# Kernel tuning notes

Hardware: AMD Instinct MI355X
Metric: run time of the kernel (lower is better)

Reference implementation:

```python
import jax, jax.numpy as jnp
import numpy as np

N = 50000   # nodes
E = 800000  # edges (avg degree 16)
F = 16      # input node feature dim
H = 64      # hidden_channels
G = 128     # number of graphs
L = 3       # num_layers
OUT = 8     # output_channels


def _glorot(key, shape):
    fan = shape[-2] + shape[-1]
    return jax.random.normal(key, shape, dtype=jnp.float32) * jnp.sqrt(2.0 / fan)


def setup_inputs() -> dict:
    key = jax.random.key(0)
    ks = jax.random.split(key, 16)
    z = lambda *s: jnp.zeros(s, jnp.float32)
    return {
        "x": jax.random.normal(ks[0], (N, F), jnp.float32),
        "pos": jax.random.normal(ks[1], (N, 3), jnp.float32),
        "edge_index": jax.random.randint(ks[2], (2, E), 0, N),
        "batch": jnp.sort(jax.random.randint(ks[3], (N,), 0, G)),
        "node_W1": _glorot(ks[4], (F, H)), "node_b1": z(H),
        "node_W2": _glorot(ks[5], (H, H)), "node_b2": z(H),
        "local_W1": _glorot(ks[6], (L, 2 * H + 3, H)), "local_b1": z(L, H),
        "local_W2": _glorot(ks[7], (L, H, H)), "local_b2": z(L, H),
        "global_W1": _glorot(ks[8], (L, H, H)), "global_b1": z(L, H),
        "global_W2": _glorot(ks[9], (L, H, H)), "global_b2": z(L, H),
        "lin1_W": _glorot(ks[10], (H, H // 2)), "lin1_b": z(H // 2),
        "lin2_W": _glorot(ks[11], (H // 2, OUT)), "lin2_b": z(OUT),
    }


def reference(x, pos, edge_index, batch,
              node_W1, node_b1, node_W2, node_b2,
              local_W1, local_b1, local_W2, local_b2,
              global_W1, global_b1, global_W2, global_b2,
              lin1_W, lin1_b, lin2_W, lin2_b):
    n = x.shape[0]
    src, dst = edge_index[0], edge_index[1]  # x_j = x[src], x_i = x[dst]
    # node_lin: Linear -> ReLU -> Linear
    h = jnp.maximum(x @ node_W1 + node_b1, 0.0) @ node_W2 + node_b2
    for l in range(L):
        # message: cat([x_i, x_j, pos_j]) -> local_nn (Linear, ReLU, Linear)
        m = jnp.concatenate([h[dst], h[src], pos[src]], axis=-1)  # [E, 2H+3]
        m = jnp.maximum(m @ local_W1[l] + local_b1[l], 0.0) @ local_W2[l] + local_b2[l]
        # aggregate: scatter-add over destination nodes
        agg = jax.ops.segment_sum(m, dst, num_segments=n)
        # global_nn (Linear, ReLU, Linear), then outer ReLU from forward loop
        h = jnp.maximum(agg @ global_W1[l] + global_b1[l], 0.0) @ global_W2[l] + global_b2[l]
        h = jnp.maximum(h, 0.0)
    h = jnp.maximum(h @ lin1_W + lin1_b, 0.0)
    out = h @ lin2_W + lin2_b  # [N, OUT]
    # graph readout: scatter-add over batch ids
    return jax.ops.segment_sum(out, batch, num_segments=G)  # [G, OUT]
```

## Files before the change

kernel.cpp:

```cpp
#include <hip/hip_runtime.h>

#define N_NODES 50000
#define N_EDGES 800000
#define NGRAPH  128
#define XPITCH  72
#define NB      391
#define HEPB    4096
#define SEPB    8192
#define NGRP    3125
#define STRIDE  64
#define SENT    N_NODES

typedef short bf16x8 __attribute__((ext_vector_type(8)));
typedef float f32x4  __attribute__((ext_vector_type(4)));


__device__ __forceinline__ float atomAddF(float* p, float v) {
#if defined(__gfx950__) || defined(__AMDGCN__)
    return unsafeAtomicAdd(p, v);
#else
    return atomicAdd(p, v);
#endif
}

__device__ __forceinline__ unsigned short f2bf(float x) {
    unsigned u = __builtin_bit_cast(unsigned, x);
    u += 0x7fffu + ((u >> 16) & 1u);
    return (unsigned short)(u >> 16);
}
__device__ __forceinline__ float bf2f(unsigned short h) {
    return __builtin_bit_cast(float, (unsigned)h << 16);
}

__device__ __forceinline__ f32x4 mk4(float b) { f32x4 a = {b, b, b, b}; return a; }

template<int NKC, int KROW>
__device__ __forceinline__ f32x4 w_tile(const bf16x8* a,
                                        const unsigned short* __restrict__ Wm,
                                        int nt, int col, int quad, f32x4 acc) {
    const unsigned short* wp = Wm + (nt * 16 + col) * KROW + quad * 8;
#pragma unroll
    for (int c = 0; c < NKC; ++c) {
        bf16x8 b = *(const bf16x8*)(wp + c * 32);
        acc = __builtin_amdgcn_mfma_f32_16x16x32_bf16(a[c], b, acc, 0, 0, 0);
    }
    return acc;
}

template<int NKC>
__device__ __forceinline__ void a_load(const unsigned short* __restrict__ sl,
                                       int col, int quad, bf16x8* a) {
    a[0] = *(const bf16x8*)(sl + col * XPITCH + quad * 8);
    if (NKC > 1) a[1] = *(const bf16x8*)(sl + col * XPITCH + quad * 8 + 32);
}

__device__ __forceinline__ void w_store1(unsigned short* __restrict__ sl,
                                         int wv, int col, int quad, f32x4 acc,
                                         bool relu) {
#pragma unroll
    for (int r = 0; r < 4; ++r) {
        float x = acc[r];
        if (relu) x = fmaxf(x, 0.f);
        sl[(quad * 4 + r) * XPITCH + wv * 16 + col] = f2bf(x);
    }
}

__device__ __forceinline__ void g_store1(unsigned short* __restrict__ g, int gn0,
                                         int wv, int col, int quad, f32x4 acc) {
#pragma unroll
    for (int r = 0; r < 4; ++r) {
        int node = gn0 + quad * 4 + r;
        if (node < N_NODES)
            g[(size_t)node * 64 + wv * 16 + col] = f2bf(acc[r]);
    }
}

__device__ __forceinline__ void wave_agg4(const int* dg, unsigned short* __restrict__ sl,
                                          const unsigned short* __restrict__ u,
                                          const unsigned short* __restrict__ vin,
                                          const unsigned short* __restrict__ srcList,
                                          int gn0, int wv, int lane) {
    int sub = lane & 15, q = lane >> 4;
    int n0 = gn0 + wv * 4;
    ushort4 uu4[4];
#pragma unroll
    for (int mi = 0; mi < 4; ++mi)
        uu4[mi] = *(const ushort4*)(u + (size_t)(n0 + mi) * 64 + sub * 4);

#pragma unroll
    for (int mi = 0; mi < 4; ++mi) {
        int m = wv * 4 + mi;
        float u0 = bf2f(uu4[mi].x), u1 = bf2f(uu4[mi].y);
        float u2 = bf2f(uu4[mi].z), u3 = bf2f(uu4[mi].w);
        int pdeg = (dg[m] + 15) & ~15;
        size_t b = (size_t)(n0 + mi) * STRIDE;
        float a0 = 0.f, a1 = 0.f, a2 = 0.f, a3 = 0.f;

        for (int g0 = 0; g0 < pdeg; g0 += 16) {
            ushort4 ss = *(const ushort4*)(srcList + b + g0 + 4 * q);
            int s0 = ss.x, s1 = ss.y, s2 = ss.z, s3 = ss.w;
            ushort4 w0 = *(const ushort4*)(vin + (size_t)s0 * 64 + sub * 4);
            ushort4 w1 = *(const ushort4*)(vin + (size_t)s1 * 64 + sub * 4);
            ushort4 w2 = *(const ushort4*)(vin + (size_t)s2 * 64 + sub * 4);
            ushort4 w3 = *(const ushort4*)(vin + (size_t)s3 * 64 + sub * 4);
            a0 += fmaxf(u0 + bf2f(w0.x), 0.f) + fmaxf(u0 + bf2f(w1.x), 0.f)
                + fmaxf(u0 + bf2f(w2.x), 0.f) + fmaxf(u0 + bf2f(w3.x), 0.f);
            a1 += fmaxf(u1 + bf2f(w0.y), 0.f) + fmaxf(u1 + bf2f(w1.y), 0.f)
                + fmaxf(u1 + bf2f(w2.y), 0.f) + fmaxf(u1 + bf2f(w3.y), 0.f);
            a2 += fmaxf(u2 + bf2f(w0.z), 0.f) + fmaxf(u2 + bf2f(w1.z), 0.f)
                + fmaxf(u2 + bf2f(w2.z), 0.f) + fmaxf(u2 + bf2f(w3.z), 0.f);
            a3 += fmaxf(u3 + bf2f(w0.w), 0.f) + fmaxf(u3 + bf2f(w1.w), 0.f)
                + fmaxf(u3 + bf2f(w2.w), 0.f) + fmaxf(u3 + bf2f(w3.w), 0.f);
        }

        a0 += __shfl_xor(a0, 16); a0 += __shfl_xor(a0, 32);
        a1 += __shfl_xor(a1, 16); a1 += __shfl_xor(a1, 32);
        a2 += __shfl_xor(a2, 16); a2 += __shfl_xor(a2, 32);
        a3 += __shfl_xor(a3, 16); a3 += __shfl_xor(a3, 32);

        if (q == 0) {
            ushort4 o;
            o.x = f2bf(a0); o.y = f2bf(a1); o.z = f2bf(a2); o.w = f2bf(a3);
            *(ushort4*)&sl[m * XPITCH + sub * 4] = o;
        }
    }
}

#define OFF_NW1T  0
#define OFF_NW2T  2048
#define OFF_LYR   6144
#define LYR_SZ    20480
#define OFF_LIN1T 67584
#define OFF_LIN2T 69632
#define WT_TOTAL  70144

__global__ __launch_bounds__(256) void kPrep(
    const float* __restrict__ nW1, const float* __restrict__ nW2,
    const float* __restrict__ lW1, const float* __restrict__ lW2,
    const float* __restrict__ gW1, const float* __restrict__ gW2,
    const float* __restrict__ lin1W, const float* __restrict__ lin2W,
    unsigned short* __restrict__ WT, int* __restrict__ gHist,
    int* __restrict__ doneCnt, float* __restrict__ out,
    unsigned short* __restrict__ v0, unsigned short* __restrict__ v1) {
    int i = blockIdx.x * 256 + threadIdx.x;
    if (blockIdx.x == 0) {
        for (int k = threadIdx.x; k < NB; k += 256) gHist[k] = 0;
        for (int k = threadIdx.x; k < NGRAPH * 8; k += 256) out[k] = 0.f;
        if (threadIdx.x == 0) *doneCnt = 0;
    }
    if (i < 64) {
        v0[(size_t)N_NODES * 64 + i] = 0xFF80;
        v1[(size_t)N_NODES * 64 + i] = 0xFF80;
    }
    if (i >= WT_TOTAL) return;
    int j = i;
    if (j < 2048) {
        int n = j >> 5, k = j & 31;
        WT[i] = (k < 16) ? f2bf(nW1[k * 64 + n]) : 0;
        return;
    }
    j -= 2048;
    if (j < 4096) {
        int n = j >> 6, k = j & 63;
        WT[i] = f2bf(nW2[k * 64 + n]);
        return;
    }
    j -= 4096;
    if (j < 3 * LYR_SZ) {
        int l = j / LYR_SZ;  j -= l * LYR_SZ;
        int m = j >> 12;     j &= 4095;
        int n = j >> 6, k = j & 63;
        const float* src;
        if (m == 0)      src = lW1 + (size_t)l * 131 * 64;
        else if (m == 1) src = lW1 + (size_t)l * 131 * 64 + 64 * 64;
        else if (m == 2) src = lW2 + (size_t)l * 4096;
        else if (m == 3) src = gW1 + (size_t)l * 4096;
        else             src = gW2 + (size_t)l * 4096;
        WT[i] = f2bf(src[k * 64 + n]);
        return;
    }
    j -= 3 * LYR_SZ;
    if (j < 2048) {
        int n = j >> 6, k = j & 63;
        WT[i] = f2bf(lin1W[k * 32 + n]);
        return;
    }
    j -= 2048;
    {
        int n = j >> 5, k = j & 31;
        WT[i] = (n < 8) ? f2bf(lin2W[k * 8 + n]) : 0;
    }
}

__global__ __launch_bounds__(256) void kHist(const int* __restrict__ ei,
                                             int* __restrict__ gHist,
                                             int* __restrict__ bucketOff,
                                             int* __restrict__ cursor,
                                             int* __restrict__ doneCnt) {
    __shared__ int h[NB];
    __shared__ int s0[512], s1[512];
    __shared__ int amLast;
    int tid = threadIdx.x;
    for (int i = tid; i < NB; i += 256) h[i] = 0;
    __syncthreads();
    int base = blockIdx.x * HEPB;
#pragma unroll
    for (int k = 0; k < HEPB; k += 256) {
        int e = base + k + tid;
        if (e < N_EDGES) atomicAdd(&h[ei[N_EDGES + e] >> 7], 1);
    }
    __syncthreads();
    for (int i = tid; i < NB; i += 256)
        if (h[i]) atomicAdd(&gHist[i], h[i]);

    __threadfence();
    if (tid == 0) amLast = (atomicAdd(doneCnt, 1) == (int)gridDim.x - 1);
    __syncthreads();
    if (!amLast) return;
    __threadfence();

    for (int e = tid; e < 512; e += 256)
        s0[e] = (e < NB) ? atomicAdd(&gHist[e], 0) : 0;
    __syncthreads();
    int* sp = s0; int* dp = s1;
    for (int off = 1; off < 512; off <<= 1) {
        for (int e = tid; e < 512; e += 256)
            dp[e] = sp[e] + ((e >= off) ? sp[e - off] : 0);
        __syncthreads();
        int* t = sp; sp = dp; dp = t;
    }
    for (int e = tid; e < NB; e += 256) {
        int cnt = atomicAdd(&gHist[e], 0);
        int excl = sp[e] - cnt;
        bucketOff[e] = excl;
        cursor[e] = excl;
    }
    if (tid == 0) bucketOff[NB] = sp[NB - 1];
}

__global__ __launch_bounds__(256) void kScat(const int* __restrict__ ei,
                                             int* __restrict__ cursor,
                                             int* __restrict__ packs) {
    __shared__ int sdata[SEPB];
    __shared__ int hist[NB];
    __shared__ int loff[NB + 1];
    __shared__ int gbase[NB];
    __shared__ int sc0[512], sc1[512];
    int tid = threadIdx.x;
    int base = blockIdx.x * SEPB;
    int nE = min(SEPB, N_EDGES - base);

    for (int i = tid; i < NB; i += 256) hist[i] = 0;
    __syncthreads();

    int myPack[SEPB / 256];
    unsigned short myRank[SEPB / 256];
#pragma unroll
    for (int kk = 0; kk < SEPB / 256; ++kk) {
        int e = base + kk * 256 + tid;
        if (e < N_EDGES) {
            int s = ei[e], d = ei[N_EDGES + e];
            myPack[kk] = (s << 16) | d;
            myRank[kk] = (unsigned short)atomicAdd(&hist[d >> 7], 1);
        }
    }
    __syncthreads();

    for (int e = tid; e < 512; e += 256) sc0[e] = (e < NB) ? hist[e] : 0;
    __syncthreads();
    int* sp = sc0; int* dp = sc1;
    for (int off = 1; off < 512; off <<= 1) {
        for (int e = tid; e < 512; e += 256)
            dp[e] = sp[e] + ((e >= off) ? sp[e - off] : 0);
        __syncthreads();
        int* t = sp; sp = dp; dp = t;
    }
    for (int e = tid; e < NB; e += 256) loff[e] = sp[e] - hist[e];
    if (tid == 0) loff[NB] = sp[NB - 1];
    __syncthreads();

    for (int e = tid; e < NB; e += 256)
        gbase[e] = hist[e] ? atomicAdd(&cursor[e], hist[e]) : 0;
#pragma unroll
    for (int kk = 0; kk < SEPB / 256; ++kk) {
        int e = base + kk * 256 + tid;
        if (e < N_EDGES) {
            int p = myPack[kk];
            int b = (p & 0xffff) >> 7;
            sdata[loff[b] + myRank[kk]] = p;
        }
    }
    __syncthreads();

    for (int i = tid; i < nE; i += 256) {
        int p = sdata[i];
        int b = (p & 0xffff) >> 7;
        packs[gbase[b] + (i - loff[b])] = p;
    }
}

__global__ __launch_bounds__(256) void kSortA(
    const int* __restrict__ bucketOff, const int* __restrict__ packs,
    unsigned short* __restrict__ srcList, int* __restrict__ degArr,
    const float* __restrict__ x, const float* __restrict__ pos,
    const unsigned short* __restrict__ WT,
    const float* __restrict__ nb1, const float* __restrict__ nb2,
    const float* __restrict__ lW1f, const float* __restrict__ lb1,
    unsigned short* __restrict__ u, unsigned short* __restrict__ v) {
    __shared__ int cur[128];
    __shared__ unsigned short SL[16 * XPITCH];
    __shared__ float pw[48];

    int tid = threadIdx.x;
    if (blockIdx.x < NB) {
        int nbk = blockIdx.x;
        int nodeBase = nbk * 128;
        int nvalid = min(128, N_NODES - nodeBase);
        int eb = bucketOff[nbk], ee = bucketOff[nbk + 1];

        if (tid < 128) cur[tid] = 0;
        __syncthreads();
        for (int i = eb + tid; i < ee; i += 256) {
            int p = packs[i];
            int node = p & 127;
            int r = atomicAdd(&cur[node], 1);
            if (r < STRIDE)
                srcList[(size_t)(nodeBase + node) * STRIDE + r] =
                    (unsigned short)(((unsigned)p) >> 16);
        }
        __syncthreads();
        if (tid < nvalid) {
            int d = min(cur[tid], STRIDE);
            degArr[nodeBase + tid] = d;
            int pd = (d + 15) & ~15;
            size_t b2 = (size_t)(nodeBase + tid) * STRIDE;
            for (int r = d; r < pd; ++r) srcList[b2 + r] = (unsigned short)SENT;
        }
        return;
    }

    int gn0 = (blockIdx.x - NB) * 16;
    int lane = tid & 63;
    int wv = __builtin_amdgcn_readfirstlane(tid >> 6);
    int col = lane & 15, quad = lane >> 4;

    for (int idx = tid; idx < 512; idx += 256) {
        int m = idx >> 5, k = idx & 31;
        int node = gn0 + m;
        float val = (k < 16) ? x[(size_t)node * 16 + k] : 0.f;
        SL[m * XPITCH + k] = f2bf(val);
    }
    if (tid < 48) {
        int node = gn0 + tid / 3;
        pw[tid] = pos[(size_t)node * 3 + tid % 3];
    }
    __syncthreads();

    bf16x8 a[2];
    f32x4 acc;

    a_load<1>(SL, col, quad, a);
    acc = w_tile<1, 32>(a, WT + OFF_NW1T, wv, col, quad, mk4(nb1[wv * 16 + col]));
    __syncthreads();
    w_store1(SL, wv, col, quad, acc, true);
    __syncthreads();

    a_load<2>(SL, col, quad, a);
    acc = w_tile<2, 64>(a, WT + OFF_NW2T, wv, col, quad, mk4(nb2[wv * 16 + col]));
    __syncthreads();
    w_store1(SL, wv, col, quad, acc, false);
    __syncthreads();

    const unsigned short* aT = WT + OFF_LYR;
    const unsigned short* bT = aT + 4096;
    const float* W1c = lW1f + 128 * 64;

    a_load<2>(SL, col, quad, a);
    acc = w_tile<2, 64>(a, aT, wv, col, quad, mk4(0.f));
    g_store1(u, gn0, wv, col, quad, acc);

    int ch = wv * 16 + col;
    acc = w_tile<2, 64>(a, bT, wv, col, quad, mk4(lb1[ch]));
    float w0 = W1c[ch], w1 = W1c[64 + ch], w2 = W1c[128 + ch];
#pragma unroll
    for (int r = 0; r < 4; ++r) {
        int rr = quad * 4 + r;
        acc[r] += pw[rr * 3 + 0] * w0 + pw[rr * 3 + 1] * w1 + pw[rr * 3 + 2] * w2;
    }
    g_store1(v, gn0, wv, col, quad, acc);
}

__global__ __launch_bounds__(256) void kB(
    const float* __restrict__ pos, const int* __restrict__ degArr,
    const unsigned short* __restrict__ srcList,
    const unsigned short* __restrict__ WT, int l,
    const float* __restrict__ lb2, const float* __restrict__ gb1,
    const float* __restrict__ gb2,
    const float* __restrict__ lW1f_next, const float* __restrict__ b1n,
    unsigned short* __restrict__ u,
    const unsigned short* __restrict__ vin,
    unsigned short* __restrict__ vout) {
    __shared__ unsigned short SL[16 * XPITCH];
    __shared__ float pw[48];
    __shared__ int dgW[16];
    int tid = threadIdx.x;
    int lane = tid & 63;
    int wv = __builtin_amdgcn_readfirstlane(tid >> 6);
    int gn0 = blockIdx.x * 16;
    int col = lane & 15, quad = lane >> 4;

    const unsigned short* LYR = WT + OFF_LYR + (size_t)l * LYR_SZ;
    const unsigned short* lW2T = LYR + 2 * 4096;
    const unsigned short* gW1T = LYR + 3 * 4096;
    const unsigned short* gW2T = LYR + 4 * 4096;
    const unsigned short* aTn = WT + OFF_LYR + (size_t)(l + 1) * LYR_SZ;
    const unsigned short* bTn = aTn + 4096;

    if (tid < 48) {
        int node = gn0 + tid / 3;
        pw[tid] = pos[(size_t)node * 3 + tid % 3];
    }
    if (tid < 16) dgW[tid] = degArr[gn0 + tid];
    __syncthreads();

    wave_agg4(dgW, SL, u, vin, srcList, gn0, wv, lane);
    __syncthreads();

    bf16x8 a[2];
    f32x4 acc;
    float dgr[4];
#pragma unroll
    for (int r = 0; r < 4; ++r) dgr[r] = (float)dgW[quad * 4 + r];

    {
        float b = lb2[wv * 16 + col];
        f32x4 init = {dgr[0] * b, dgr[1] * b, dgr[2] * b, dgr[3] * b};
        a_load<2>(SL, col, quad, a);
        acc = w_tile<2, 64>(a, lW2T, wv, col, quad, init);
    }
    __syncthreads();
    w_store1(SL, wv, col, quad, acc, false);
    __syncthreads();

    a_load<2>(SL, col, quad, a);
    acc = w_tile<2, 64>(a, gW1T, wv, col, quad, mk4(gb1[wv * 16 + col]));
    __syncthreads();
    w_store1(SL, wv, col, quad, acc, true);
    __syncthreads();

    a_load<2>(SL, col, quad, a);
    acc = w_tile<2, 64>(a, gW2T, wv, col, quad, mk4(gb2[wv * 16 + col]));
    __syncthreads();
    w_store1(SL, wv, col, quad, acc, true);
    __syncthreads();

    a_load<2>(SL, col, quad, a);
    acc = w_tile<2, 64>(a, aTn, wv, col, quad, mk4(0.f));
    g_store1(u, gn0, wv, col, quad, acc);

    const float* W1c = lW1f_next + 128 * 64;
    int ch = wv * 16 + col;
    acc = w_tile<2, 64>(a, bTn, wv, col, quad, mk4(b1n[ch]));
    float w0 = W1c[ch], w1 = W1c[64 + ch], w2 = W1c[128 + ch];
#pragma unroll
    for (int r = 0; r < 4; ++r) {
        int rr = quad * 4 + r;
        acc[r] += pw[rr * 3 + 0] * w0 + pw[rr * 3 + 1] * w1 + pw[rr * 3 + 2] * w2;
    }
    g_store1(vout, gn0, wv, col, quad, acc);
}

__global__ __launch_bounds__(256) void kC(
    const int* __restrict__ degArr, const unsigned short* __restrict__ srcList,
    const int* __restrict__ batch, const unsigned short* __restrict__ WT,
    const float* __restrict__ lb2, const float* __restrict__ gb1,
    const float* __restrict__ gb2,
    const float* __restrict__ lin1b, const float* __restrict__ lin2b,
    const unsigned short* __restrict__ u, const unsigned short* __restrict__ vin,
    float* __restrict__ out) {
    __shared__ unsigned short SL[16 * XPITCH];
    __shared__ int dgW[16];
    __shared__ int batchW[16];
    __shared__ float bins[16 * 8];
    int tid = threadIdx.x;
    int lane = tid & 63;
    int wv = __builtin_amdgcn_readfirstlane(tid >> 6);
    int gn0 = blockIdx.x * 16;
    int col = lane & 15, quad = lane >> 4;

    const unsigned short* LYR = WT + OFF_LYR + 2 * LYR_SZ;
    const unsigned short* lW2T = LYR + 2 * 4096;
    const unsigned short* gW1T = LYR + 3 * 4096;
    const unsigned short* gW2T = LYR + 4 * 4096;
    const unsigned short* lin1T = WT + OFF_LIN1T;
    const unsigned short* lin2T = WT + OFF_LIN2T;

    if (tid < 16) dgW[tid] = degArr[gn0 + tid];
    if (tid >= 32 && tid < 48) batchW[tid - 32] = batch[gn0 + tid - 32];
    if (tid >= 128 && tid < 256) bins[tid - 128] = 0.f;
    __syncthreads();

    wave_agg4(dgW, SL, u, vin, srcList, gn0, wv, lane);
    __syncthreads();

    bf16x8 a[2];
    f32x4 acc;
    float dgr[4];
#pragma unroll
    for (int r = 0; r < 4; ++r) dgr[r] = (float)dgW[quad * 4 + r];

    {
        float b = lb2[wv * 16 + col];
        f32x4 init = {dgr[0] * b, dgr[1] * b, dgr[2] * b, dgr[3] * b};
        a_load<2>(SL, col, quad, a);
        acc = w_tile<2, 64>(a, lW2T, wv, col, quad, init);
    }
    __syncthreads();
    w_store1(SL, wv, col, quad, acc, false);
    __syncthreads();

    a_load<2>(SL, col, quad, a);
    acc = w_tile<2, 64>(a, gW1T, wv, col, quad, mk4(gb1[wv * 16 + col]));
    __syncthreads();
    w_store1(SL, wv, col, quad, acc, true);
    __syncthreads();

    a_load<2>(SL, col, quad, a);
    acc = w_tile<2, 64>(a, gW2T, wv, col, quad, mk4(gb2[wv * 16 + col]));
    __syncthreads();
    w_store1(SL, wv, col, quad, acc, true);
    __syncthreads();

    a_load<2>(SL, col, quad, a);
    if (wv < 2)
        acc = w_tile<2, 64>(a, lin1T, wv, col, quad, mk4(lin1b[wv * 16 + col]));
    __syncthreads();
    if (wv < 2) w_store1(SL, wv, col, quad, acc, true);
    __syncthreads();

    if (wv == 0) {
        a_load<1>(SL, col, quad, a);
        f32x4 o = w_tile<1, 32>(a, lin2T, 0, col, quad,
                                mk4(col < 8 ? lin2b[col] : 0.f));
        int gmin = batchW[0];
        if (col < 8) {
#pragma unroll
            for (int r = 0; r < 4; ++r) {
                int nl = quad * 4 + r;
                atomicAdd(&bins[(batchW[nl] - gmin) * 8 + col], o[r]);
            }
        }
    }
    __syncthreads();
    int gmin = batchW[0];
    int nb8 = (batchW[15] - gmin + 1) * 8;
    for (int idx = tid; idx < nb8; idx += 256)
        atomAddF(&out[gmin * 8 + idx], bins[idx]);
}

extern "C" void kernel_launch(void* const* d_in, const int* in_sizes, int n_in,
                              void* d_out, int out_size, void* d_ws, size_t ws_size,
                              hipStream_t stream) {
    const float* x     = (const float*)d_in[0];
    const float* pos   = (const float*)d_in[1];
    const int*   ei    = (const int*)d_in[2];
    const int*   batch = (const int*)d_in[3];
    const float* nW1   = (const float*)d_in[4];
    const float* nb1   = (const float*)d_in[5];
    const float* nW2   = (const float*)d_in[6];
    const float* nb2   = (const float*)d_in[7];
    const float* lW1   = (const float*)d_in[8];
    const float* lb1   = (const float*)d_in[9];
    const float* lW2   = (const float*)d_in[10];
    const float* lb2   = (const float*)d_in[11];
    const float* gW1   = (const float*)d_in[12];
    const float* gb1   = (const float*)d_in[13];
    const float* gW2   = (const float*)d_in[14];
    const float* gb2   = (const float*)d_in[15];
    const float* lin1W = (const float*)d_in[16];
    const float* lin1b = (const float*)d_in[17];
    const float* lin2W = (const float*)d_in[18];
    const float* lin2b = (const float*)d_in[19];
    float* out = (float*)d_out;

    unsigned short* u  = (unsigned short*)d_ws;
    unsigned short* v0 = u + (size_t)N_NODES * 64;
    unsigned short* v1 = v0 + (size_t)(N_NODES + 1) * 64;
    unsigned short* WT = v1 + (size_t)(N_NODES + 1) * 64;
    int* gHist = (int*)(WT + WT_TOTAL);
    int* bucketOff = gHist + NB;
    int* cursor = bucketOff + NB + 1;
    int* doneCnt = cursor + NB;
    int* degArr = doneCnt + 1;
    int* packs = degArr + N_NODES;
    unsigned short* srcList = (unsigned short*)(packs + N_EDGES);

    kPrep<<<(WT_TOTAL + 255) / 256, 256, 0, stream>>>(nW1, nW2, lW1, lW2, gW1, gW2,
                                                      lin1W, lin2W, WT, gHist,
                                                      doneCnt, out, v0, v1);
    kHist<<<(N_EDGES + HEPB - 1) / HEPB, 256, 0, stream>>>(ei, gHist, bucketOff,
                                                           cursor, doneCnt);
    kScat<<<(N_EDGES + SEPB - 1) / SEPB, 256, 0, stream>>>(ei, cursor, packs);
    kSortA<<<NB + NGRP, 256, 0, stream>>>(bucketOff, packs, srcList, degArr,
                                          x, pos, WT, nb1, nb2, lW1, lb1, u, v0);

    kB<<<NGRP, 256, 0, stream>>>(
        pos, degArr, srcList, WT, 0,
        lb2 + 0, gb1 + 0, gb2 + 0,
        lW1 + (size_t)1 * 131 * 64, lb1 + 64,
        u, v0, v1);
    kB<<<NGRP, 256, 0, stream>>>(
        pos, degArr, srcList, WT, 1,
        lb2 + 64, gb1 + 64, gb2 + 64,
        lW1 + (size_t)2 * 131 * 64, lb1 + 128,
        u, v1, v0);
    kC<<<NGRP, 256, 0, stream>>>(
        degArr, srcList, batch, WT,
        lb2 + 128, gb1 + 128, gb2 + 128, lin1b, lin2b,
        u, v0, out);
}
```

Before: 257.2 us.

## Interleave neighbor gathers across four nodes and ping-pong shared tiles

The per-wave aggregation loop now walks the edge groups of its four destination nodes together, issuing all source-index and feature loads for those nodes before accumulating. This raises memory-level parallelism on the random gathers that dominate the edge stage. Separately, the shared activation tile is double-buffered so each MLP layer writes into the other buffer, which removes one barrier per layer. The cost is more registers for the 4x4 load array, possible lower occupancy, and extra iterations where nodes of unequal degree are masked off.

```diff
diff --git a/kernel.cpp b/kernel.cpp
--- a/kernel.cpp
+++ b/kernel.cpp
@@ -82,46 +82,59 @@
                                           int gn0, int wv, int lane) {
     int sub = lane & 15, q = lane >> 4;
     int n0 = gn0 + wv * 4;
-    ushort4 uu4[4];
-#pragma unroll
-    for (int mi = 0; mi < 4; ++mi)
-        uu4[mi] = *(const ushort4*)(u + (size_t)(n0 + mi) * 64 + sub * 4);
-
+    float uf[4][4], ac[4][4];
+    int pd[4];
+    int pdMax = 0;
 #pragma unroll
     for (int mi = 0; mi < 4; ++mi) {
-        int m = wv * 4 + mi;
-        float u0 = bf2f(uu4[mi].x), u1 = bf2f(uu4[mi].y);
-        float u2 = bf2f(uu4[mi].z), u3 = bf2f(uu4[mi].w);
-        int pdeg = (dg[m] + 15) & ~15;
-        size_t b = (size_t)(n0 + mi) * STRIDE;
-        float a0 = 0.f, a1 = 0.f, a2 = 0.f, a3 = 0.f;
-
-        for (int g0 = 0; g0 < pdeg; g0 += 16) {
-            ushort4 ss = *(const ushort4*)(srcList + b + g0 + 4 * q);
-            int s0 = ss.x, s1 = ss.y, s2 = ss.z, s3 = ss.w;
-            ushort4 w0 = *(const ushort4*)(vin + (size_t)s0 * 64 + sub * 4);
-            ushort4 w1 = *(const ushort4*)(vin + (size_t)s1 * 64 + sub * 4);
-            ushort4 w2 = *(const ushort4*)(vin + (size_t)s2 * 64 + sub * 4);
-            ushort4 w3 = *(const ushort4*)(vin + (size_t)s3 * 64 + sub * 4);
-            a0 += fmaxf(u0 + bf2f(w0.x), 0.f) + fmaxf(u0 + bf2f(w1.x), 0.f)
-                + fmaxf(u0 + bf2f(w2.x), 0.f) + fmaxf(u0 + bf2f(w3.x), 0.f);
-            a1 += fmaxf(u1 + bf2f(w0.y), 0.f) + fmaxf(u1 + bf2f(w1.y), 0.f)
-                + fmaxf(u1 + bf2f(w2.y), 0.f) + fmaxf(u1 + bf2f(w3.y), 0.f);
-            a2 += fmaxf(u2 + bf2f(w0.z), 0.f) + fmaxf(u2 + bf2f(w1.z), 0.f)
-                + fmaxf(u2 + bf2f(w2.z), 0.f) + fmaxf(u2 + bf2f(w3.z), 0.f);
-            a3 += fmaxf(u3 + bf2f(w0.w), 0.f) + fmaxf(u3 + bf2f(w1.w), 0.f)
-                + fmaxf(u3 + bf2f(w2.w), 0.f) + fmaxf(u3 + bf2f(w3.w), 0.f);
+        ushort4 uu = *(const ushort4*)(u + (size_t)(n0 + mi) * 64 + sub * 4);
+        uf[mi][0] = bf2f(uu.x); uf[mi][1] = bf2f(uu.y);
+        uf[mi][2] = bf2f(uu.z); uf[mi][3] = bf2f(uu.w);
+        pd[mi] = (dg[wv * 4 + mi] + 15) & ~15;
+        pdMax = max(pdMax, pd[mi]);
+        ac[mi][0] = ac[mi][1] = ac[mi][2] = ac[mi][3] = 0.f;
+    }
+
+    for (int g0 = 0; g0 < pdMax; g0 += 16) {
+        ushort4 ss[4];
+        ushort4 w[4][4];
+#pragma unroll
+        for (int mi = 0; mi < 4; ++mi)
+            if (g0 < pd[mi])
+                ss[mi] = *(const ushort4*)(srcList + (size_t)(n0 + mi) * STRIDE + g0 + 4 * q);
+#pragma unroll
+        for (int mi = 0; mi < 4; ++mi)
+            if (g0 < pd[mi]) {
+                w[mi][0] = *(const ushort4*)(vin + (size_t)ss[mi].x * 64 + sub * 4);
+                w[mi][1] = *(const ushort4*)(vin + (size_t)ss[mi].y * 64 + sub * 4);
+                w[mi][2] = *(const ushort4*)(vin + (size_t)ss[mi].z * 64 + sub * 4);
+                w[mi][3] = *(const ushort4*)(vin + (size_t)ss[mi].w * 64 + sub * 4);
+            }
+#pragma unroll
+        for (int mi = 0; mi < 4; ++mi)
+            if (g0 < pd[mi]) {
+#pragma unroll
+                for (int j = 0; j < 4; ++j) {
+                    ac[mi][0] += fmaxf(uf[mi][0] + bf2f(w[mi][j].x), 0.f);
+                    ac[mi][1] += fmaxf(uf[mi][1] + bf2f(w[mi][j].y), 0.f);
+                    ac[mi][2] += fmaxf(uf[mi][2] + bf2f(w[mi][j].z), 0.f);
+                    ac[mi][3] += fmaxf(uf[mi][3] + bf2f(w[mi][j].w), 0.f);
+                }
+            }
+    }
+
+#pragma unroll
+    for (int mi = 0; mi < 4; ++mi) {
+#pragma unroll
+        for (int c = 0; c < 4; ++c) {
+            ac[mi][c] += __shfl_xor(ac[mi][c], 16);
+            ac[mi][c] += __shfl_xor(ac[mi][c], 32);
         }
-
-        a0 += __shfl_xor(a0, 16); a0 += __shfl_xor(a0, 32);
-        a1 += __shfl_xor(a1, 16); a1 += __shfl_xor(a1, 32);
-        a2 += __shfl_xor(a2, 16); a2 += __shfl_xor(a2, 32);
-        a3 += __shfl_xor(a3, 16); a3 += __shfl_xor(a3, 32);
-
         if (q == 0) {
             ushort4 o;
-            o.x = f2bf(a0); o.y = f2bf(a1); o.z = f2bf(a2); o.w = f2bf(a3);
-            *(ushort4*)&sl[m * XPITCH + sub * 4] = o;
+            o.x = f2bf(ac[mi][0]); o.y = f2bf(ac[mi][1]);
+            o.z = f2bf(ac[mi][2]); o.w = f2bf(ac[mi][3]);
+            *(ushort4*)&sl[(wv * 4 + mi) * XPITCH + sub * 4] = o;
         }
     }
 }
@@ -308,7 +321,7 @@
     const float* __restrict__ lW1f, const float* __restrict__ lb1,
     unsigned short* __restrict__ u, unsigned short* __restrict__ v) {
     __shared__ int cur[128];
-    __shared__ unsigned short SL[16 * XPITCH];
+    __shared__ unsigned short SL[2][16 * XPITCH];
     __shared__ float pw[48];
 
     int tid = threadIdx.x;
@@ -348,7 +361,7 @@
         int m = idx >> 5, k = idx & 31;
         int node = gn0 + m;
         float val = (k < 16) ? x[(size_t)node * 16 + k] : 0.f;
-        SL[m * XPITCH + k] = f2bf(val);
+        SL[0][m * XPITCH + k] = f2bf(val);
     }
     if (tid < 48) {
         int node = gn0 + tid / 3;
@@ -359,23 +372,21 @@
     bf16x8 a[2];
     f32x4 acc;
 
-    a_load<1>(SL, col, quad, a);
+    a_load<1>(SL[0], col, quad, a);
     acc = w_tile<1, 32>(a, WT + OFF_NW1T, wv, col, quad, mk4(nb1[wv * 16 + col]));
-    __syncthreads();
-    w_store1(SL, wv, col, quad, acc, true);
-    __syncthreads();
-
-    a_load<2>(SL, col, quad, a);
+    w_store1(SL[1], wv, col, quad, acc, true);
+    __syncthreads();
+
+    a_load<2>(SL[1], col, quad, a);
     acc = w_tile<2, 64>(a, WT + OFF_NW2T, wv, col, quad, mk4(nb2[wv * 16 + col]));
-    __syncthreads();
-    w_store1(SL, wv, col, quad, acc, false);
+    w_store1(SL[0], wv, col, quad, acc, false);
     __syncthreads();
 
     const unsigned short* aT = WT + OFF_LYR;
     const unsigned short* bT = aT + 4096;
     const float* W1c = lW1f + 128 * 64;
 
-    a_load<2>(SL, col, quad, a);
+    a_load<2>(SL[0], col, quad, a);
     acc = w_tile<2, 64>(a, aT, wv, col, quad, mk4(0.f));
     g_store1(u, gn0, wv, col, quad, acc);
 
@@ -400,7 +411,7 @@
     unsigned short* __restrict__ u,
     const unsigned short* __restrict__ vin,
     unsigned short* __restrict__ vout) {
-    __shared__ unsigned short SL[16 * XPITCH];
+    __shared__ unsigned short SL[2][16 * XPITCH];
     __shared__ float pw[48];
     __shared__ int dgW[16];
     int tid = threadIdx.x;
@@ -423,7 +434,7 @@
     if (tid < 16) dgW[tid] = degArr[gn0 + tid];
     __syncthreads();
 
-    wave_agg4(dgW, SL, u, vin, srcList, gn0, wv, lane);
+    wave_agg4(dgW, SL[0], u, vin, srcList, gn0, wv, lane);
     __syncthreads();
 
     bf16x8 a[2];
@@ -435,26 +446,23 @@
     {
         float b = lb2[wv * 16 + col];
         f32x4 init = {dgr[0] * b, dgr[1] * b, dgr[2] * b, dgr[3] * b};
-        a_load<2>(SL, col, quad, a);
+        a_load<2>(SL[0], col, quad, a);
         acc = w_tile<2, 64>(a, lW2T, wv, col, quad, init);
     }
-    __syncthreads();
-    w_store1(SL, wv, col, quad, acc, false);
-    __syncthreads();
-
-    a_load<2>(SL, col, quad, a);
+    w_store1(SL[1], wv, col, quad, acc, false);
+    __syncthreads();
+
+    a_load<2>(SL[1], col, quad, a);
     acc = w_tile<2, 64>(a, gW1T, wv, col, quad, mk4(gb1[wv * 16 + col]));
-    __syncthreads();
-    w_store1(SL, wv, col, quad, acc, true);
-    __syncthreads();
-
-    a_load<2>(SL, col, quad, a);
+    w_store1(SL[0], wv, col, quad, acc, true);
+    __syncthreads();
+
+    a_load<2>(SL[0], col, quad, a);
     acc = w_tile<2, 64>(a, gW2T, wv, col, quad, mk4(gb2[wv * 16 + col]));
-    __syncthreads();
-    w_store1(SL, wv, col, quad, acc, true);
-    __syncthreads();
-
-    a_load<2>(SL, col, quad, a);
+    w_store1(SL[1], wv, col, quad, acc, true);
+    __syncthreads();
+
+    a_load<2>(SL[1], col, quad, a);
     acc = w_tile<2, 64>(a, aTn, wv, col, quad, mk4(0.f));
     g_store1(u, gn0, wv, col, quad, acc);
 
@@ -478,7 +486,7 @@
     const float* __restrict__ lin1b, const float* __restrict__ lin2b,
     const unsigned short* __restrict__ u, const unsigned short* __restrict__ vin,
     float* __restrict__ out) {
-    __shared__ unsigned short SL[16 * XPITCH];
+    __shared__ unsigned short SL[2][16 * XPITCH];
     __shared__ int dgW[16];
     __shared__ int batchW[16];
     __shared__ float bins[16 * 8];
@@ -500,7 +508,7 @@
     if (tid >= 128 && tid < 256) bins[tid - 128] = 0.f;
     __syncthreads();
 
-    wave_agg4(dgW, SL, u, vin, srcList, gn0, wv, lane);
+    wave_agg4(dgW, SL[0], u, vin, srcList, gn0, wv, lane);
     __syncthreads();
 
     bf16x8 a[2];
@@ -512,34 +520,31 @@
     {
         float b = lb2[wv * 16 + col];
         f32x4 init = {dgr[0] * b, dgr[1] * b, dgr[2] * b, dgr[3] * b};
-        a_load<2>(SL, col, quad, a);
+        a_load<2>(SL[0], col, quad, a);
         acc = w_tile<2, 64>(a, lW2T, wv, col, quad, init);
     }
-    __syncthreads();
-    w_store1(SL, wv, col, quad, acc, false);
-    __syncthreads();
-
-    a_load<2>(SL, col, quad, a);
+    w_store1(SL[1], wv, col, quad, acc, false);
+    __syncthreads();
+
+    a_load<2>(SL[1], col, quad, a);
     acc = w_tile<2, 64>(a, gW1T, wv, col, quad, mk4(gb1[wv * 16 + col]));
-    __syncthreads();
-    w_store1(SL, wv, col, quad, acc, true);
-    __syncthreads();
-
-    a_load<2>(SL, col, quad, a);
+    w_store1(SL[0], wv, col, quad, acc, true);
+    __syncthreads();
+
+    a_load<2>(SL[0], col, quad, a);
     acc = w_tile<2, 64>(a, gW2T, wv, col, quad, mk4(gb2[wv * 16 + col]));
-    __syncthreads();
-    w_store1(SL, wv, col, quad, acc, true);
-    __syncthreads();
-
-    a_load<2>(SL, col, quad, a);
-    if (wv < 2)
+    w_store1(SL[1], wv, col, quad, acc, true);
+    __syncthreads();
+
+    a_load<2>(SL[1], col, quad, a);
+    if (wv < 2) {
         acc = w_tile<2, 64>(a, lin1T, wv, col, quad, mk4(lin1b[wv * 16 + col]));
-    __syncthreads();
-    if (wv < 2) w_store1(SL, wv, col, quad, acc, true);
+        w_store1(SL[0], wv, col, quad, acc, true);
+    }
     __syncthreads();
 
     if (wv == 0) {
-        a_load<1>(SL, col, quad, a);
+        a_load<1>(SL[0], col, quad, a);
         f32x4 o = w_tile<1, 32>(a, lin2T, 0, col, quad,
                                 mk4(col < 8 ? lin2b[col] : 0.f));
         int gmin = batchW[0];
```

After: 279.3 us. 8.6% more time.

## Pre-fold consecutive linear layers without activation into combined weights

Applied to the files above, without the earlier changes.

Exploits the absence of a nonlinearity between node_W2 and the first message layer, and between local_W2 and global_W1 (linear commutes with segment-sum), by multiplying those weight pairs together in a prep kernel. The folded biases are precomputed too, including the degree-scaled local bias. Each node-tile kernel drops one 64x64 MFMA GEMM stage plus its LDS store and barriers. The cost is extra serial fp32 matmul work in kPrep on 5 extra blocks, and different bf16 rounding since the product is quantised once.

```diff
diff --git a/kernel.cpp b/kernel.cpp
--- a/kernel.cpp
+++ b/kernel.cpp
@@ -10,6 +10,7 @@
 #define NGRP    3125
 #define STRIDE  64
 #define SENT    N_NODES
+#define PREP_BLKS 275
 
 typedef short bf16x8 __attribute__((ext_vector_type(8)));
 typedef float f32x4  __attribute__((ext_vector_type(4)));
@@ -139,14 +140,55 @@
     const float* __restrict__ lW1, const float* __restrict__ lW2,
     const float* __restrict__ gW1, const float* __restrict__ gW2,
     const float* __restrict__ lin1W, const float* __restrict__ lin2W,
-    unsigned short* __restrict__ WT, int* __restrict__ gHist,
-    int* __restrict__ doneCnt, float* __restrict__ out,
+    const float* __restrict__ nb2, const float* __restrict__ lb1,
+    const float* __restrict__ lb2,
+    unsigned short* __restrict__ WT, float* __restrict__ fb,
+    int* __restrict__ gHist, int* __restrict__ doneCnt,
+    float* __restrict__ out,
     unsigned short* __restrict__ v0, unsigned short* __restrict__ v1) {
-    int i = blockIdx.x * 256 + threadIdx.x;
+    int tid = threadIdx.x;
+    if (blockIdx.x >= PREP_BLKS) {
+        int f = blockIdx.x - PREP_BLKS;
+        const float* Wl;
+        const float* Wr;
+        size_t slot;
+        if (f == 0)      { Wl = nW2;          Wr = lW1;            slot = OFF_LYR; }
+        else if (f == 1) { Wl = nW2;          Wr = lW1 + 64 * 64;  slot = OFF_LYR + 4096; }
+        else { int l = f - 2;
+               Wl = lW2 + (size_t)l * 4096;   Wr = gW1 + (size_t)l * 4096;
+               slot = OFF_LYR + (size_t)l * LYR_SZ + 2 * 4096; }
+        for (int o = tid; o < 4096; o += 256) {
+            int n = o >> 6, kk = o & 63;
+            float s = 0.f;
+            for (int t = 0; t < 64; ++t)
+                s += Wl[kk * 64 + t] * Wr[t * 64 + n];
+            WT[slot + (size_t)n * 64 + kk] = f2bf(s);
+        }
+        if (tid < 64) {
+            if (f == 0) {
+                float s = 0.f;
+                for (int t = 0; t < 64; ++t) s += nb2[t] * lW1[t * 64 + tid];
+                fb[tid] = s;
+            } else if (f == 1) {
+                float s = 0.f;
+                for (int t = 0; t < 64; ++t) s += nb2[t] * lW1[(64 + t) * 64 + tid];
+                fb[64 + tid] = s + lb1[tid];
+            } else {
+                int l = f - 2;
+                float s = 0.f;
+                for (int t = 0; t < 64; ++t)
+                    s += lb2[l * 64 + t] * gW1[(size_t)l * 4096 + t * 64 + tid];
+                fb[128 + l * 64 + tid] = s;
+            }
+        }
+        return;
+    }
+
+    int i = blockIdx.x * 256 + tid;
     if (blockIdx.x == 0) {
-        for (int k = threadIdx.x; k < NB; k += 256) gHist[k] = 0;
-        for (int k = threadIdx.x; k < NGRAPH * 8; k += 256) out[k] = 0.f;
-        if (threadIdx.x == 0) *doneCnt = 0;
+        for (int k = tid; k < NB; k += 256) gHist[k] = 0;
+        for (int k = tid; k < NGRAPH * 8; k += 256) out[k] = 0.f;
+        if (tid == 0) *doneCnt = 0;
     }
     if (i < 64) {
         v0[(size_t)N_NODES * 64 + i] = 0xFF80;
@@ -160,21 +202,16 @@
         return;
     }
     j -= 2048;
-    if (j < 4096) {
-        int n = j >> 6, k = j & 63;
-        WT[i] = f2bf(nW2[k * 64 + n]);
-        return;
-    }
+    if (j < 4096) return;
     j -= 4096;
     if (j < 3 * LYR_SZ) {
         int l = j / LYR_SZ;  j -= l * LYR_SZ;
         int m = j >> 12;     j &= 4095;
+        if (m == 2 || m == 3 || (l == 0 && m < 2)) return;
         int n = j >> 6, k = j & 63;
         const float* src;
         if (m == 0)      src = lW1 + (size_t)l * 131 * 64;
         else if (m == 1) src = lW1 + (size_t)l * 131 * 64 + 64 * 64;
-        else if (m == 2) src = lW2 + (size_t)l * 4096;
-        else if (m == 3) src = gW1 + (size_t)l * 4096;
         else             src = gW2 + (size_t)l * 4096;
         WT[i] = f2bf(src[k * 64 + n]);
         return;
@@ -303,9 +340,9 @@
     const int* __restrict__ bucketOff, const int* __restrict__ packs,
     unsigned short* __restrict__ srcList, int* __restrict__ degArr,
     const float* __restrict__ x, const float* __restrict__ pos,
-    const unsigned short* __restrict__ WT,
-    const float* __restrict__ nb1, const float* __restrict__ nb2,
-    const float* __restrict__ lW1f, const float* __restrict__ lb1,
+    const unsigned short* __restrict__ WT, const float* __restrict__ fb,
+    const float* __restrict__ nb1,
+    const float* __restrict__ lW1f,
     unsigned short* __restrict__ u, unsigned short* __restrict__ v) {
     __shared__ int cur[128];
     __shared__ unsigned short SL[16 * XPITCH];
@@ -365,22 +402,16 @@
     w_store1(SL, wv, col, quad, acc, true);
     __syncthreads();
 
+    const unsigned short* FA = WT + OFF_LYR;
+    const unsigned short* FB = FA + 4096;
+    const float* W1c = lW1f + 128 * 64;
+    int ch = wv * 16 + col;
+
     a_load<2>(SL, col, quad, a);
-    acc = w_tile<2, 64>(a, WT + OFF_NW2T, wv, col, quad, mk4(nb2[wv * 16 + col]));
-    __syncthreads();
-    w_store1(SL, wv, col, quad, acc, false);
-    __syncthreads();
-
-    const unsigned short* aT = WT + OFF_LYR;
-    const unsigned short* bT = aT + 4096;
-    const float* W1c = lW1f + 128 * 64;
-
-    a_load<2>(SL, col, quad, a);
-    acc = w_tile<2, 64>(a, aT, wv, col, quad, mk4(0.f));
+    acc = w_tile<2, 64>(a, FA, wv, col, quad, mk4(fb[ch]));
     g_store1(u, gn0, wv, col, quad, acc);
 
-    int ch = wv * 16 + col;
-    acc = w_tile<2, 64>(a, bT, wv, col, quad, mk4(lb1[ch]));
+    acc = w_tile<2, 64>(a, FB, wv, col, quad, mk4(fb[64 + ch]));
     float w0 = W1c[ch], w1 = W1c[64 + ch], w2 = W1c[128 + ch];
 #pragma unroll
     for (int r = 0; r < 4; ++r) {
@@ -393,9 +424,8 @@
 __global__ __launch_bounds__(256) void kB(
     const float* __restrict__ pos, const int* __restrict__ degArr,
     const unsigned short* __restrict__ srcList,
-    const unsigned short* __restrict__ WT, int l,
-    const float* __restrict__ lb2, const float* __restrict__ gb1,
-    const float* __restrict__ gb2,
+    const unsigned short* __restrict__ WT, const float* __restrict__ fb, int l,
+    const float* __restrict__ gb1, const float* __restrict__ gb2,
     const float* __restrict__ lW1f_next, const float* __restrict__ b1n,
     unsigned short* __restrict__ u,
     const unsigned short* __restrict__ vin,
@@ -410,11 +440,11 @@
     int col = lane & 15, quad = lane >> 4;
 
     const unsigned short* LYR = WT + OFF_LYR + (size_t)l * LYR_SZ;
-    const unsigned short* lW2T = LYR + 2 * 4096;
-    const unsigned short* gW1T = LYR + 3 * 4096;
+    const unsigned short* GT   = LYR + 2 * 4096;
     const unsigned short* gW2T = LYR + 4 * 4096;
     const unsigned short* aTn = WT + OFF_LYR + (size_t)(l + 1) * LYR_SZ;
     const unsigned short* bTn = aTn + 4096;
+    const float* lbg = fb + 128 + l * 64;
 
     if (tid < 48) {
         int node = gn0 + tid / 3;
@@ -432,24 +462,21 @@
 #pragma unroll
     for (int r = 0; r < 4; ++r) dgr[r] = (float)dgW[quad * 4 + r];
 
+    int ch = wv * 16 + col;
     {
-        float b = lb2[wv * 16 + col];
-        f32x4 init = {dgr[0] * b, dgr[1] * b, dgr[2] * b, dgr[3] * b};
+        float bb = lbg[ch];
+        float g1 = gb1[ch];
+        f32x4 init = {dgr[0] * bb + g1, dgr[1] * bb + g1,
+                      dgr[2] * bb + g1, dgr[3] * bb + g1};
         a_load<2>(SL, col, quad, a);
-        acc = w_tile<2, 64>(a, lW2T, wv, col, quad, init);
-    }
-    __syncthreads();
-    w_store1(SL, wv, col, quad, acc, false);
+        acc = w_tile<2, 64>(a, GT, wv, col, quad, init);
+    }
+    __syncthreads();
+    w_store1(SL, wv, col, quad, acc, true);
     __syncthreads();
 
     a_load<2>(SL, col, quad, a);
-    acc = w_tile<2, 64>(a, gW1T, wv, col, quad, mk4(gb1[wv * 16 + col]));
-    __syncthreads();
-    w_store1(SL, wv, col, quad, acc, true);
-    __syncthreads();
-
-    a_load<2>(SL, col, quad, a);
-    acc = w_tile<2, 64>(a, gW2T, wv, col, quad, mk4(gb2[wv * 16 + col]));
+    acc = w_tile<2, 64>(a, gW2T, wv, col, quad, mk4(gb2[ch]));
     __syncthreads();
     w_store1(SL, wv, col, quad, acc, true);
     __syncthreads();
@@ -459,7 +486,6 @@
     g_store1(u, gn0, wv, col, quad, acc);
 
     const float* W1c = lW1f_next + 128 * 64;
-    int ch = wv * 16 + col;
     acc = w_tile<2, 64>(a, bTn, wv, col, quad, mk4(b1n[ch]));
     float w0 = W1c[ch], w1 = W1c[64 + ch], w2 = W1c[128 + ch];
 #pragma unroll
@@ -473,8 +499,8 @@
 __global__ __launch_bounds__(256) void kC(
     const int* __restrict__ degArr, const unsigned short* __restrict__ srcList,
     const int* __restrict__ batch, const unsigned short* __restrict__ WT,
-    const float* __restrict__ lb2, const float* __restrict__ gb1,
-    const float* __restrict__ gb2,
+    const float* __restrict__ fb,
+    const float* __restrict__ gb1, const float* __restrict__ gb2,
     const float* __restrict__ lin1b, const float* __restrict__ lin2b,
     const unsigned short* __restrict__ u, const unsigned short* __restrict__ vin,
     float* __restrict__ out) {
@@ -489,11 +515,11 @@
     int col = lane & 15, quad = lane >> 4;
 
     const unsigned short* LYR = WT + OFF_LYR + 2 * LYR_SZ;
-    const unsigned short* lW2T = LYR + 2 * 4096;
-    const unsigned short* gW1T = LYR + 3 * 4096;
+    const unsigned short* GT   = LYR + 2 * 4096;
     const unsigned short* gW2T = LYR + 4 * 4096;
     const unsigned short* lin1T = WT + OFF_LIN1T;
     const unsigned short* lin2T = WT + OFF_LIN2T;
+    const float* lbg = fb + 128 + 2 * 64;
 
     if (tid < 16) dgW[tid] = degArr[gn0 + tid];
     if (tid >= 32 && tid < 48) batchW[tid - 32] = batch[gn0 + tid - 32];
@@ -509,24 +535,21 @@
 #pragma unroll
     for (int r = 0; r < 4; ++r) dgr[r] = (float)dgW[quad * 4 + r];
 
+    int ch = wv * 16 + col;
     {
-        float b = lb2[wv * 16 + col];
-        f32x4 init = {dgr[0] * b, dgr[1] * b, dgr[2] * b, dgr[3] * b};
+        float bb = lbg[ch];
+        float g1 = gb1[ch];
+        f32x4 init = {dgr[0] * bb + g1, dgr[1] * bb + g1,
+                      dgr[2] * bb + g1, dgr[3] * bb + g1};
         a_load<2>(SL, col, quad, a);
-        acc = w_tile<2, 64>(a, lW2T, wv, col, quad, init);
-    }
-    __syncthreads();
-    w_store1(SL, wv, col, quad, acc, false);
+        acc = w_tile<2, 64>(a, GT, wv, col, quad, init);
+    }
+    __syncthreads();
+    w_store1(SL, wv, col, quad, acc, true);
     __syncthreads();
 
     a_load<2>(SL, col, quad, a);
-    acc = w_tile<2, 64>(a, gW1T, wv, col, quad, mk4(gb1[wv * 16 + col]));
-    __syncthreads();
-    w_store1(SL, wv, col, quad, acc, true);
-    __syncthreads();
-
-    a_load<2>(SL, col, quad, a);
-    acc = w_tile<2, 64>(a, gW2T, wv, col, quad, mk4(gb2[wv * 16 + col]));
+    acc = w_tile<2, 64>(a, gW2T, wv, col, quad, mk4(gb2[ch]));
     __syncthreads();
     w_store1(SL, wv, col, quad, acc, true);
     __syncthreads();
@@ -592,30 +615,32 @@
     int* cursor = bucketOff + NB + 1;
     int* doneCnt = cursor + NB;
     int* degArr = doneCnt + 1;
-    int* packs = degArr + N_NODES;
+    float* fbias = (float*)(degArr + N_NODES);
+    int* packs = (int*)(fbias + 320);
     unsigned short* srcList = (unsigned short*)(packs + N_EDGES);
 
-    kPrep<<<(WT_TOTAL + 255) / 256, 256, 0, stream>>>(nW1, nW2, lW1, lW2, gW1, gW2,
-                                                      lin1W, lin2W, WT, gHist,
-                                                      doneCnt, out, v0, v1);
+    kPrep<<<PREP_BLKS + 5, 256, 0, stream>>>(nW1, nW2, lW1, lW2, gW1, gW2,
+                                             lin1W, lin2W, nb2, lb1, lb2,
+                                             WT, fbias, gHist, doneCnt, out,
+                                             v0, v1);
     kHist<<<(N_EDGES + HEPB - 1) / HEPB, 256, 0, stream>>>(ei, gHist, bucketOff,
                                                            cursor, doneCnt);
     kScat<<<(N_EDGES + SEPB - 1) / SEPB, 256, 0, stream>>>(ei, cursor, packs);
     kSortA<<<NB + NGRP, 256, 0, stream>>>(bucketOff, packs, srcList, degArr,
-                                          x, pos, WT, nb1, nb2, lW1, lb1, u, v0);
+                                          x, pos, WT, fbias, nb1, lW1, u, v0);
 
     kB<<<NGRP, 256, 0, stream>>>(
-        pos, degArr, srcList, WT, 0,
-        lb2 + 0, gb1 + 0, gb2 + 0,
+        pos, degArr, srcList, WT, fbias, 0,
+        gb1 + 0, gb2 + 0,
         lW1 + (size_t)1 * 131 * 64, lb1 + 64,
         u, v0, v1);
     kB<<<NGRP, 256, 0, stream>>>(
-        pos, degArr, srcList, WT, 1,
-        lb2 + 64, gb1 + 64, gb2 + 64,
+        pos, degArr, srcList, WT, fbias, 1,
+        gb1 + 64, gb2 + 64,
         lW1 + (size_t)2 * 131 * 64, lb1 + 128,
         u, v1, v0);
     kC<<<NGRP, 256, 0, stream>>>(
-        degArr, srcList, batch, WT,
-        lb2 + 128, gb1 + 128, gb2 + 128, lin1b, lin2b,
+        degArr, srcList, batch, WT, fbias,
+        gb1 + 128, gb2 + 128, lin1b, lin2b,
         u, v0, out);
 }
```

New measurement: 283.7 us. 10.3% more time.
